# Optimization experiments

Hardware: AMD Instinct MI355X
Metric: run time of the kernel (lower is better)

Reference implementation:

```python
import jax, jax.numpy as jnp
import numpy as np

E = 500000       # num edges == num lane rows (per-edge lane gathers)
NUM_VEH = 2048   # number of actor nodes
D = 64           # v_dim == out_dim
H = 4            # num attention heads
EA = 2           # edge_attr_dim


def setup_inputs() -> dict:
    key = jax.random.key(0)
    ks = jax.random.split(key, 12)
    lane_actor_index = jnp.stack([
        jax.random.randint(ks[2], (E,), 0, E),        # src: index into lane_vectors
        jax.random.randint(ks[3], (E,), 0, NUM_VEH),  # tgt: actor index
    ]).astype(jnp.int64)
    return {
        "lane_vectors": jax.random.normal(ks[0], (E, 2), jnp.float32),
        "rotate_imat": jax.random.normal(ks[1], (NUM_VEH, 2, 2), jnp.float32),
        "lane_actor_index": lane_actor_index,
        "lane_actor_attr": jax.random.normal(ks[4], (E, EA), jnp.float32),
        "v_enc": jax.random.normal(ks[5], (NUM_VEH, D), jnp.float32),
        "mlp_w1": jax.random.normal(ks[6], (2, D), jnp.float32) * (1.0 / np.sqrt(2.0)),
        "mlp_b1": jnp.zeros((D,), jnp.float32),
        "mlp_w2": jax.random.normal(ks[7], (D, D), jnp.float32) * (1.0 / np.sqrt(D)),
        "mlp_b2": jnp.zeros((D,), jnp.float32),
        "Wh": jax.random.normal(ks[8], (H, D, D), jnp.float32) * (1.0 / np.sqrt(D)),
        "ah": jax.random.normal(ks[9], (H, 2 * D + EA), jnp.float32) * (1.0 / np.sqrt(2 * D + EA)),
        "out_w": jax.random.normal(ks[10], (H * D, D), jnp.float32) * (1.0 / np.sqrt(H * D)),
    }


def reference(lane_vectors, rotate_imat, lane_actor_index, lane_actor_attr,
              v_enc, mlp_w1, mlp_b1, mlp_w2, mlp_b2, Wh, ah, out_w):
    src, tgt = lane_actor_index[0], lane_actor_index[1]
    num_veh = v_enc.shape[0]
    d = Wh.shape[2]

    # per-edge lane vector rotated into each actor frame: [E, 2]
    lane = jnp.einsum('ei,eij->ej', lane_vectors[src], rotate_imat[tgt])
    # lane embedding MLP -> [E, D]
    lane_enc = jax.nn.relu(lane @ mlp_w1 + mlp_b1) @ mlp_w2 + mlp_b2
    # joint node features: actors first, then per-edge lane rows  [num_veh+E, D]
    x = jnp.concatenate([v_enc, lane_enc], axis=0)

    def head(W, a):
        h = x @ W                         # [num_veh+E, D]
        h_lane = h[num_veh:]              # [E, D] (per-edge source features)
        h_tgt = h[:num_veh][tgt]          # [E, D] (gathered target features)
        a_src, a_tgt, a_attr = a[:d], a[d:2 * d], a[2 * d:]
        # a([h_lane, h_tgt, attr]) decomposed to avoid materializing the concat
        score = jax.nn.leaky_relu(h_lane @ a_src + h_tgt @ a_tgt + lane_actor_attr @ a_attr)
        score = score - jnp.max(score)    # global max-subtract as in source
        ex = jnp.exp(score)
        den = jax.ops.segment_sum(ex, tgt, num_segments=num_veh)[tgt]
        attn = ex / (den + 1e-16)
        out = jax.ops.segment_sum(h_lane * attn[:, None], tgt, num_segments=num_veh)
        return jax.nn.elu(out)            # [num_veh, D]

    outs = jax.vmap(head)(Wh, ah)                         # [H, num_veh, D]
    out = jnp.transpose(outs, (1, 0, 2)).reshape(num_veh, -1)  # [num_veh, H*D]
    out = jax.nn.elu(out)
    return out @ out_w                                    # [num_veh, D]
```

## Files before the change

kernel.cpp:

```cpp
#include <hip/hip_runtime.h>
#include <math.h>

#define E_EDGES 500000
#define NV 2048
#define DIM 64
#define NH 4
#define NSH 16
#define NSH2 8
#define SCAP 80
#define CAP (NSH2 * SCAP)
#define TP 17
#define NBE ((E_EDGES + 255) / 256)

__device__ __forceinline__ float elu1(float x) { return x > 0.f ? x : expm1f(x); }

__device__ __forceinline__ void prep_body(
        const float* __restrict__ Wh, const float* __restrict__ ah,
        const float* __restrict__ w1, const float* __restrict__ b1,
        const float* __restrict__ w2, const float* __restrict__ b2,
        float* __restrict__ atp, float* __restrict__ aattr,
        float* __restrict__ pkw, float* __restrict__ bconst,
        float* s_asp) {
    int tid = threadIdx.x;
    int h = tid >> 6, i = tid & 63;
    const float* W = Wh + h * DIM * DIM + i * DIM;
    const float* a = ah + h * 130;
    float s0 = 0.f, s1 = 0.f;
    for (int j = 0; j < DIM; j++) {
        s0 = fmaf(W[j], a[j], s0);
        s1 = fmaf(W[j], a[DIM + j], s1);
    }
    s_asp[tid] = s0;
    atp[tid] = s1;
    if (tid < 2 * NH) aattr[tid] = ah[(tid >> 1) * 130 + 2 * DIM + (tid & 1)];
    __syncthreads();
    float ws = 0.f;
    for (int d = 0; d < DIM; d++) ws = fmaf(w2[i * DIM + d], s_asp[h * DIM + d], ws);
    pkw[8 * i + 4 + h] = ws;
    if (h == 0) {
        pkw[8 * i + 0] = w1[i];
        pkw[8 * i + 1] = w1[DIM + i];
        pkw[8 * i + 2] = b1[i];
        pkw[8 * i + 3] = 0.f;
    }
    if (i == 0) {
        float bc = 0.f;
        for (int d = 0; d < DIM; d++) bc = fmaf(b2[d], s_asp[h * DIM + d], bc);
        bconst[h] = bc;
    }
}

__global__ void k_prep(const float* __restrict__ Wh, const float* __restrict__ ah,
                       const float* __restrict__ w1, const float* __restrict__ b1,
                       const float* __restrict__ w2, const float* __restrict__ b2,
                       float* __restrict__ atp, float* __restrict__ aattr,
                       float* __restrict__ pkw, float* __restrict__ bconst) {
    __shared__ float s_asp[NH * DIM];
    prep_body(Wh, ah, w1, b1, w2, b2, atp, aattr, pkw, bconst, s_asp);
}

__global__ void k_scatter_prep(const int* __restrict__ idx, const float* __restrict__ lv,
                               const float* __restrict__ attr, const float* __restrict__ rot,
                               int* __restrict__ run2, float4* __restrict__ packed,
                               const float* __restrict__ Wh, const float* __restrict__ ah,
                               const float* __restrict__ w1, const float* __restrict__ b1,
                               const float* __restrict__ w2, const float* __restrict__ b2,
                               float* __restrict__ atp, float* __restrict__ aattr,
                               float* __restrict__ pkw, float* __restrict__ bconst) {
    __shared__ float s_asp[NH * DIM];
    if (blockIdx.x == NBE) {
        prep_body(Wh, ah, w1, b1, w2, b2, atp, aattr, pkw, bconst, s_asp);
        return;
    }
    int e = blockIdx.x * blockDim.x + threadIdx.x;
    if (e < E_EDGES) {
        int sh = blockIdx.x & (NSH2 - 1);
        int t = idx[E_EDGES + e];
        int s = idx[e];
        float l0 = lv[2 * s], l1 = lv[2 * s + 1];
        float4 R = *(const float4*)&rot[t * 4];
        float p0 = l0 * R.x + l1 * R.z;
        float p1 = l0 * R.y + l1 * R.w;
        float a0 = attr[2 * e], a1 = attr[2 * e + 1];
        int p = atomicAdd(&run2[sh * NV + t], 1);
        if (p < SCAP) packed[(size_t)t * CAP + sh * SCAP + p] = make_float4(p0, p1, a0, a1);
    }
}

__global__ void k_hist(const int* __restrict__ idx, int* __restrict__ cnt) {
    int e = blockIdx.x * blockDim.x + threadIdx.x;
    if (e < E_EDGES) {
        int sh = blockIdx.x & (NSH - 1);
        atomicAdd(&cnt[sh * NV + idx[E_EDGES + e]], 1);
    }
}

__global__ void k_scan(const int* __restrict__ cnt, int* __restrict__ offs, int* __restrict__ run) {
    __shared__ int a[NV], b[NV];
    int tid = threadIdx.x;
    int tot[2];
    for (int ii = 0; ii < 2; ii++) {
        int t = tid + ii * 1024;
        int s0 = 0;
        for (int s = 0; s < NSH; s++) s0 += cnt[s * NV + t];
        tot[ii] = s0;
        a[t] = s0;
    }
    __syncthreads();
    int* cur = a;
    int* nxt = b;
    for (int off = 1; off < NV; off <<= 1) {
        for (int ii = 0; ii < 2; ii++) {
            int i = tid + ii * 1024;
            int v = cur[i];
            if (i >= off) v += cur[i - off];
            nxt[i] = v;
        }
        __syncthreads();
        int* tmp = cur; cur = nxt; nxt = tmp;
    }
    for (int ii = 0; ii < 2; ii++) {
        int i = tid + ii * 1024;
        int incl = cur[i];
        offs[i + 1] = incl;
        int base = incl - tot[ii];
        for (int s = 0; s < NSH; s++) {
            run[s * NV + i] = base;
            base += cnt[s * NV + i];
        }
    }
    if (tid == 0) offs[0] = 0;
}

__global__ void k_scatter_sorted(const int* __restrict__ idx, const float* __restrict__ lv,
                                 const float* __restrict__ attr, const float* __restrict__ rot,
                                 int* __restrict__ run, float4* __restrict__ packed) {
    int e = blockIdx.x * blockDim.x + threadIdx.x;
    if (e < E_EDGES) {
        int sh = blockIdx.x & (NSH - 1);
        int t = idx[E_EDGES + e];
        int s = idx[e];
        float l0 = lv[2 * s], l1 = lv[2 * s + 1];
        float4 R = *(const float4*)&rot[t * 4];
        float p0 = l0 * R.x + l1 * R.z;
        float p1 = l0 * R.y + l1 * R.w;
        float a0 = attr[2 * e], a1 = attr[2 * e + 1];
        int p = atomicAdd(&run[sh * NV + t], 1);
        packed[p] = make_float4(p0, p1, a0, a1);
    }
}

__launch_bounds__(256, 4)
__global__ void k_main(const float4* __restrict__ packed, const int* __restrict__ offs,
                       const int* __restrict__ run2, int mode,
                       const float* __restrict__ pkw, const float* __restrict__ bconst,
                       const float* __restrict__ atp, const float* __restrict__ aattr,
                       const float* __restrict__ venc,
                       const float* __restrict__ w2, const float* __restrict__ b2,
                       const float* __restrict__ Wh, const float* __restrict__ ow,
                       float* __restrict__ out) {
    __shared__ float tile[4][64 * TP];
    __shared__ float s_exq[4][4 * 72];
    __shared__ float s_den[4 * NH];
    __shared__ float s_G[NH * DIM];
    __shared__ float s_dfin[NH];
    __shared__ float s_vec[NH * DIM];
    __shared__ float s_z[NH * DIM];
    __shared__ float s_part[4][DIM];
    __shared__ int s_seg[NSH2];
    __shared__ int s_pre[NSH2 + 1];

    int t = blockIdx.x;
    int tid = threadIdx.x;
    int w = tid >> 6, lane = tid & 63;
    int q = lane >> 4, dm = lane & 15;

    int start = 0, cntT;
    if (mode) {
        if (tid < NSH2) s_seg[tid] = min(run2[tid * NV + t], SCAP);
        __syncthreads();
        if (tid == 0) {
            int acc = 0;
            s_pre[0] = 0;
            #pragma unroll
            for (int j = 0; j < NSH2; j++) { acc += s_seg[j]; s_pre[j + 1] = acc; }
        }
        __syncthreads();
        cntT = s_pre[NSH2];
    } else {
        start = offs[t];
        cntT = offs[t + 1] - start;
    }

    float xv = venc[t * DIM + lane];
    float tsv[NH];
    #pragma unroll
    for (int h = 0; h < NH; h++) {
        float v = xv * atp[h * DIM + lane];
        #pragma unroll
        for (int m = 32; m >= 1; m >>= 1) v += __shfl_xor(v, m, 64);
        tsv[h] = v + bconst[h];
    }

    float aat[2 * NH];
    #pragma unroll
    for (int i = 0; i < 2 * NH; i++) aat[i] = aattr[i];

    float gacc[4][NH];
    float dacc[NH] = {0.f, 0.f, 0.f, 0.f};
    #pragma unroll
    for (int c = 0; c < 4; c++)
        #pragma unroll
        for (int h = 0; h < NH; h++) gacc[c][h] = 0.f;

    float* tw = &tile[w][0];
    const float4* pk4 = (const float4*)pkw;

    for (int base = w * 64; base < cntT; base += 256) {
        int r = base + lane;
        bool act = r < cntT;
        float4 pd = make_float4(0.f, 0.f, 0.f, 0.f);
        if (act) {
            int addr;
            if (mode) {
                int sh = 0;
                #pragma unroll
                for (int j = 1; j < NSH2; j++) sh += (r >= s_pre[j]) ? 1 : 0;
                addr = t * CAP + sh * SCAP + (r - s_pre[sh]);
            } else {
                addr = start + r;
            }
            pd = packed[addr];
        }
        float p0 = pd.x, p1 = pd.y, a0 = pd.z, a1 = pd.w;

        float sc0 = fmaf(a1, aat[1], fmaf(a0, aat[0], tsv[0]));
        float sc1 = fmaf(a1, aat[3], fmaf(a0, aat[2], tsv[1]));
        float sc2 = fmaf(a1, aat[5], fmaf(a0, aat[4], tsv[2]));
        float sc3 = fmaf(a1, aat[7], fmaf(a0, aat[6], tsv[3]));

        #pragma unroll
        for (int k = 0; k < DIM; k++) {
            float4 cA = pk4[2 * k];
            float4 cB = pk4[2 * k + 1];
            float hk = fmaxf(fmaf(p1, cA.y, fmaf(p0, cA.x, cA.z)), 0.f);
            sc0 = fmaf(hk, cB.x, sc0);
            sc1 = fmaf(hk, cB.y, sc1);
            sc2 = fmaf(hk, cB.z, sc2);
            sc3 = fmaf(hk, cB.w, sc3);
        }

        sc0 = sc0 > 0.f ? sc0 : 0.01f * sc0;
        sc1 = sc1 > 0.f ? sc1 : 0.01f * sc1;
        sc2 = sc2 > 0.f ? sc2 : 0.01f * sc2;
        sc3 = sc3 > 0.f ? sc3 : 0.01f * sc3;
        float ex0 = act ? __expf(sc0) : 0.f;
        float ex1 = act ? __expf(sc1) : 0.f;
        float ex2 = act ? __expf(sc2) : 0.f;
        float ex3 = act ? __expf(sc3) : 0.f;
        dacc[0] += ex0; dacc[1] += ex1; dacc[2] += ex2; dacc[3] += ex3;

        *(float4*)&s_exq[w][q * 72 + dm * 4] = make_float4(ex0, ex1, ex2, ex3);

        const float4* exq = (const float4*)&s_exq[w][q * 72];
        #pragma unroll
        for (int c = 0; c < 4; c++) {
            #pragma unroll
            for (int kk = 0; kk < 16; kk++) {
                float4 cA = pk4[2 * (c * 16 + kk)];
                float hk = fmaxf(fmaf(p1, cA.y, fmaf(p0, cA.x, cA.z)), 0.f);
                tw[lane * TP + kk] = hk;
            }
            asm volatile("s_waitcnt lgkmcnt(0)" ::: "memory");
            __builtin_amdgcn_sched_barrier(0);
            for (int s = 0; s < 16; s++) {
                int S = q * 16 + s;
                float le = tw[S * TP + dm];
                float4 e4 = exq[s];
                gacc[c][0] = fmaf(e4.x, le, gacc[c][0]);
                gacc[c][1] = fmaf(e4.y, le, gacc[c][1]);
                gacc[c][2] = fmaf(e4.z, le, gacc[c][2]);
                gacc[c][3] = fmaf(e4.w, le, gacc[c][3]);
            }
            asm volatile("s_waitcnt lgkmcnt(0)" ::: "memory");
            __builtin_amdgcn_sched_barrier(0);
        }
    }

    #pragma unroll
    for (int c = 0; c < 4; c++)
        #pragma unroll
        for (int h = 0; h < NH; h++) tw[(c * 4 + h) * 64 + lane] = gacc[c][h];
    #pragma unroll
    for (int h = 0; h < NH; h++) {
        float v = dacc[h];
        #pragma unroll
        for (int m = 32; m >= 1; m >>= 1) v += __shfl_xor(v, m, 64);
        if (lane == 0) s_den[w * NH + h] = v;
    }
    __syncthreads();

    {
        int hh = tid >> 6, k = tid & 63, c = k >> 4, dmo = k & 15;
        float sum = 0.f;
        #pragma unroll
        for (int wv = 0; wv < 4; wv++) {
            const float* tp = &tile[wv][0];
            #pragma unroll
            for (int qi = 0; qi < 4; qi++) sum += tp[(c * 4 + hh) * 64 + qi * 16 + dmo];
        }
        s_G[tid] = sum;
    }
    if (tid < NH) {
        s_dfin[tid] = s_den[tid] + s_den[NH + tid] + s_den[2 * NH + tid] + s_den[3 * NH + tid];
    }
    __syncthreads();

    int hh = tid >> 6, d = tid & 63;

    {
        float df = s_dfin[hh];
        float acc = b2[d] * df;
        for (int k = 0; k < DIM; k++)
            acc = fmaf(w2[k * DIM + d], s_G[hh * DIM + k], acc);
        s_vec[tid] = acc / (df + 1e-16f);
    }
    __syncthreads();

    {
        float acc = 0.f;
        for (int i = 0; i < DIM; i++)
            acc = fmaf(s_vec[hh * DIM + i], Wh[hh * DIM * DIM + i * DIM + d], acc);
        s_z[tid] = elu1(elu1(acc));
    }
    __syncthreads();

    {
        float part = 0.f;
        for (int kk = 0; kk < 64; kk++)
            part = fmaf(s_z[hh * 64 + kk], ow[(hh * 64 + kk) * DIM + d], part);
        s_part[hh][d] = part;
    }
    __syncthreads();
    if (tid < DIM)
        out[t * DIM + tid] = s_part[0][tid] + s_part[1][tid] + s_part[2][tid] + s_part[3][tid];
}

extern "C" void kernel_launch(void* const* d_in, const int* in_sizes, int n_in,
                              void* d_out, int out_size, void* d_ws, size_t ws_size,
                              hipStream_t stream) {
    const float* lv   = (const float*)d_in[0];
    const float* rot  = (const float*)d_in[1];
    const int*   idx  = (const int*)d_in[2];
    const float* attr = (const float*)d_in[3];
    const float* venc = (const float*)d_in[4];
    const float* w1   = (const float*)d_in[5];
    const float* b1   = (const float*)d_in[6];
    const float* w2   = (const float*)d_in[7];
    const float* b2   = (const float*)d_in[8];
    const float* Wh   = (const float*)d_in[9];
    const float* ah   = (const float*)d_in[10];
    const float* ow   = (const float*)d_in[11];
    float* out = (float*)d_out;

    size_t direct_need = (size_t)NV * CAP * 16 + (size_t)NSH2 * NV * 4 + 65536;

    if (ws_size >= direct_need) {
        char* p = (char*)d_ws;
        float4* packed = (float4*)p;  p += (size_t)NV * CAP * 16;
        int* run2   = (int*)p;   p += NSH2 * NV * 4;
        float* atp    = (float*)p; p += NH * DIM * 4;
        float* aattr  = (float*)p; p += 16 * 4;
        float* pkw    = (float*)p; p += DIM * 8 * 4;
        float* bconst = (float*)p; p += 8 * 4;

        hipMemsetAsync(run2, 0, NSH2 * NV * 4, stream);
        hipLaunchKernelGGL(k_scatter_prep, dim3(NBE + 1), dim3(256), 0, stream,
                           idx, lv, attr, rot, run2, packed,
                           Wh, ah, w1, b1, w2, b2, atp, aattr, pkw, bconst);
        hipLaunchKernelGGL(k_main, dim3(NV), dim3(256), 0, stream,
                           packed, (const int*)run2 , run2, 1,
                           pkw, bconst, atp, aattr, venc, w2, b2, Wh, ow, out);
    } else {
        char* p = (char*)d_ws;
        float4* packed = (float4*)p;  p += (size_t)E_EDGES * 16;
        int* cnt    = (int*)p;   p += NSH * NV * 4;
        int* offs   = (int*)p;   p += (NV + 4) * 4;
        int* run    = (int*)p;   p += NSH * NV * 4;
        float* atp    = (float*)p; p += NH * DIM * 4;
        float* aattr  = (float*)p; p += 16 * 4;
        float* pkw    = (float*)p; p += DIM * 8 * 4;
        float* bconst = (float*)p; p += 8 * 4;

        hipMemsetAsync(cnt, 0, NSH * NV * 4, stream);
        hipLaunchKernelGGL(k_prep, dim3(1), dim3(256), 0, stream,
                           Wh, ah, w1, b1, w2, b2, atp, aattr, pkw, bconst);
        hipLaunchKernelGGL(k_hist, dim3(NBE), dim3(256), 0, stream, idx, cnt);
        hipLaunchKernelGGL(k_scan, dim3(1), dim3(1024), 0, stream, cnt, offs, run);
        hipLaunchKernelGGL(k_scatter_sorted, dim3(NBE), dim3(256), 0, stream,
                           idx, lv, attr, rot, run, packed);
        hipLaunchKernelGGL(k_main, dim3(NV), dim3(256), 0, stream,
                           packed, offs, run, 0,
                           pkw, bconst, atp, aattr, venc, w2, b2, Wh, ow, out);
    }
}
```

Baseline: 94.38 us.

## Replace LDS tile transpose with readlane broadcast for per-lane hidden accumulation

Result: slower. 132.7 us (+40.6%).

```diff
diff --git a/kernel.cpp b/kernel.cpp
--- a/kernel.cpp
+++ b/kernel.cpp
@@ -9,10 +9,12 @@
 #define NSH2 8
 #define SCAP 80
 #define CAP (NSH2 * SCAP)
-#define TP 17
 #define NBE ((E_EDGES + 255) / 256)
 
 __device__ __forceinline__ float elu1(float x) { return x > 0.f ? x : expm1f(x); }
+__device__ __forceinline__ float rdlane(float v, int j) {
+    return __uint_as_float(__builtin_amdgcn_readlane(__float_as_uint(v), j));
+}
 
 __device__ __forceinline__ void prep_body(
         const float* __restrict__ Wh, const float* __restrict__ ah,
@@ -159,8 +161,7 @@
                        const float* __restrict__ w2, const float* __restrict__ b2,
                        const float* __restrict__ Wh, const float* __restrict__ ow,
                        float* __restrict__ out) {
-    __shared__ float tile[4][64 * TP];
-    __shared__ float s_exq[4][4 * 72];
+    __shared__ float s_Gw[4][NH][DIM];
     __shared__ float s_den[4 * NH];
     __shared__ float s_G[NH * DIM];
     __shared__ float s_dfin[NH];
@@ -173,7 +174,6 @@
     int t = blockIdx.x;
     int tid = threadIdx.x;
     int w = tid >> 6, lane = tid & 63;
-    int q = lane >> 4, dm = lane & 15;
 
     int start = 0, cntT;
     if (mode) {
@@ -206,15 +206,16 @@
     #pragma unroll
     for (int i = 0; i < 2 * NH; i++) aat[i] = aattr[i];
 
-    float gacc[4][NH];
+    const float4* pk4 = (const float4*)pkw;
+
+    float w1a, w1b, b1l;
+    {
+        float4 cA = pk4[2 * lane];
+        w1a = cA.x; w1b = cA.y; b1l = cA.z;
+    }
+
+    float gacc[NH] = {0.f, 0.f, 0.f, 0.f};
     float dacc[NH] = {0.f, 0.f, 0.f, 0.f};
-    #pragma unroll
-    for (int c = 0; c < 4; c++)
-        #pragma unroll
-        for (int h = 0; h < NH; h++) gacc[c][h] = 0.f;
-
-    float* tw = &tile[w][0];
-    const float4* pk4 = (const float4*)pkw;
 
     for (int base = w * 64; base < cntT; base += 256) {
         int r = base + lane;
@@ -260,37 +261,24 @@
         float ex3 = act ? __expf(sc3) : 0.f;
         dacc[0] += ex0; dacc[1] += ex1; dacc[2] += ex2; dacc[3] += ex3;
 
-        *(float4*)&s_exq[w][q * 72 + dm * 4] = make_float4(ex0, ex1, ex2, ex3);
-
-        const float4* exq = (const float4*)&s_exq[w][q * 72];
         #pragma unroll
-        for (int c = 0; c < 4; c++) {
-            #pragma unroll
-            for (int kk = 0; kk < 16; kk++) {
-                float4 cA = pk4[2 * (c * 16 + kk)];
-                float hk = fmaxf(fmaf(p1, cA.y, fmaf(p0, cA.x, cA.z)), 0.f);
-                tw[lane * TP + kk] = hk;
-            }
-            asm volatile("s_waitcnt lgkmcnt(0)" ::: "memory");
-            __builtin_amdgcn_sched_barrier(0);
-            for (int s = 0; s < 16; s++) {
-                int S = q * 16 + s;
-                float le = tw[S * TP + dm];
-                float4 e4 = exq[s];
-                gacc[c][0] = fmaf(e4.x, le, gacc[c][0]);
-                gacc[c][1] = fmaf(e4.y, le, gacc[c][1]);
-                gacc[c][2] = fmaf(e4.z, le, gacc[c][2]);
-                gacc[c][3] = fmaf(e4.w, le, gacc[c][3]);
-            }
-            asm volatile("s_waitcnt lgkmcnt(0)" ::: "memory");
-            __builtin_amdgcn_sched_barrier(0);
+        for (int j = 0; j < 64; j++) {
+            float p0j = rdlane(p0, j);
+            float p1j = rdlane(p1, j);
+            float e0j = rdlane(ex0, j);
+            float e1j = rdlane(ex1, j);
+            float e2j = rdlane(ex2, j);
+            float e3j = rdlane(ex3, j);
+            float hk = fmaxf(fmaf(p1j, w1b, fmaf(p0j, w1a, b1l)), 0.f);
+            gacc[0] = fmaf(e0j, hk, gacc[0]);
+            gacc[1] = fmaf(e1j, hk, gacc[1]);
+            gacc[2] = fmaf(e2j, hk, gacc[2]);
+            gacc[3] = fmaf(e3j, hk, gacc[3]);
         }
     }
 
     #pragma unroll
-    for (int c = 0; c < 4; c++)
-        #pragma unroll
-        for (int h = 0; h < NH; h++) tw[(c * 4 + h) * 64 + lane] = gacc[c][h];
+    for (int h = 0; h < NH; h++) s_Gw[w][h][lane] = gacc[h];
     #pragma unroll
     for (int h = 0; h < NH; h++) {
         float v = dacc[h];
@@ -300,23 +288,13 @@
     }
     __syncthreads();
 
-    {
-        int hh = tid >> 6, k = tid & 63, c = k >> 4, dmo = k & 15;
-        float sum = 0.f;
-        #pragma unroll
-        for (int wv = 0; wv < 4; wv++) {
-            const float* tp = &tile[wv][0];
-            #pragma unroll
-            for (int qi = 0; qi < 4; qi++) sum += tp[(c * 4 + hh) * 64 + qi * 16 + dmo];
-        }
-        s_G[tid] = sum;
-    }
+    int hh = tid >> 6, d = tid & 63;
+
+    s_G[tid] = s_Gw[0][hh][d] + s_Gw[1][hh][d] + s_Gw[2][hh][d] + s_Gw[3][hh][d];
     if (tid < NH) {
         s_dfin[tid] = s_den[tid] + s_den[NH + tid] + s_den[2 * NH + tid] + s_den[3 * NH + tid];
     }
     __syncthreads();
-
-    int hh = tid >> 6, d = tid & 63;
 
     {
         float df = s_dfin[hh];
```
